# Kernel tuning notes

Measured on AMD Instinct MI355X. Metric: run time of the kernel, lower is better.

The kernel has to match this reference:

```python
import jax, jax.numpy as jnp
import numpy as np
from jax import lax

B, L, H = 256, 256, 128
K_MIN, K_MAX, ITERS = 2, 8, 3
ALPHA, BETA = 0.5, 0.5
EPS8, EPS9 = 1e-8, 1e-9


def setup_inputs() -> dict:
    key = jax.random.key(0)
    k1, k2, k3 = jax.random.split(key, 3)
    user_features = jax.random.normal(k1, (B, L, H), dtype=jnp.float32)
    W = jax.random.normal(k2, (H, H), dtype=jnp.float32) * (1.0 / np.sqrt(H))
    b_init = jax.random.normal(k3, (B, K_MAX, L), dtype=jnp.float32)
    return {"user_features": user_features, "W": W, "b_init": b_init}


def _cap_scale(cap):
    # squash-style scalar: n/(1+n)/sqrt(n+eps), n = ||cap||^2
    n = jnp.sum(cap * cap, axis=-1, keepdims=True)
    return n / (1.0 + n) / jnp.sqrt(n + EPS9)


def reference(user_features, W, b_init):
    e = user_features                                  # [B,L,H]
    hat = e @ W.T                                      # nn.Linear(H,H,bias=False)
    # repeat over capsules then transpose -> every capsule sees same projection
    hat_k = jnp.broadcast_to(hat[:, None, :, :], (B, K_MAX, L, H))
    hat_iter = lax.stop_gradient(hat_k)                # stop_grad=True path

    b = b_init
    cap = None
    c = None
    for t in range(ITERS):
        c = jax.nn.softmax(b, axis=-1)                 # mask is all ones
        if t < ITERS - 1:
            cap = jnp.einsum('bkl,bklh->bkh', c, hat_iter)
            cap = _cap_scale(cap) * cap
            delta = jnp.einsum('bklh,bkh->bkl', hat_iter, cap)
            b = b + delta
        else:
            cap = jnp.einsum('bkl,bklh->bkh', c, hat_k)
            cap = _cap_scale(cap) * cap
    interest_capsule = cap                             # [B,K,H]
    final_c = c                                        # [B,K,L]

    e_norm = e / (jnp.linalg.norm(e, axis=-1, keepdims=True) + EPS8)
    strength = jnp.linalg.norm(interest_capsule, axis=-1)  # [B,K]

    scores = []
    for k in range(K_MIN, K_MAX + 1):
        _, idx = lax.top_k(strength, k)                # [B,k]
        c_k = jnp.take_along_axis(final_c, idx[:, :, None], axis=1)  # [B,k,L]
        denom = c_k.sum(axis=-1, keepdims=True) + EPS8
        mu_k = jnp.einsum('bkl,blh->bkh', c_k, e) / denom
        mu_n = mu_k / (jnp.linalg.norm(mu_k, axis=-1, keepdims=True) + EPS8)
        cos = jnp.einsum('blh,bkh->bkl', e_norm, mu_n)
        consistency = (c_k * cos).sum(axis=(-1, -2)) / float(max(1, k) * max(1, L))
        if k > 1:
            pair = jnp.einsum('bkh,bjh->bkj', mu_n, mu_n)
            upper = jnp.triu(pair, k=1).sum(axis=(-1, -2))
            diversity = 1.0 - (2.0 / (k * (k - 1))) * upper
        else:
            diversity = jnp.ones((B,), dtype=mu_n.dtype)
        scores.append(ALPHA * consistency + BETA * diversity)

    k_scores = jnp.stack(scores, axis=1)               # [B, K_MAX-K_MIN+1]
    optimal_k = jnp.argmax(k_scores, axis=1) + K_MIN   # [B]
    return optimal_k, k_scores
```

## Files before the change

### kernel.cpp

```cpp
#include <hip/hip_runtime.h>
#include <hip/hip_bf16.h>
#include <math.h>

#define NB 256
#define NL 256
#define NH 128
#define NK 8

typedef __attribute__((ext_vector_type(8))) short bf16x8;
typedef __attribute__((ext_vector_type(4))) short s16x4;
typedef __attribute__((ext_vector_type(4))) float f32x4;

static __device__ __forceinline__ short f2bf(float x) {
    __hip_bfloat16 b = __float2bfloat16(x);
    return *reinterpret_cast<short*>(&b);
}
static __device__ __forceinline__ float bf2f(short s) {
    union { unsigned int u; float f; } v;
    v.u = ((unsigned int)(unsigned short)s) << 16;
    return v.f;
}

#define CTI(l, k) ((l) * 12 + ((((l) >> 5) & 7) << 2) + (k))
#define MFMA __builtin_amdgcn_mfma_f32_16x16x32_bf16

__global__ __launch_bounds__(256) void setup_w_kernel(const float* __restrict__ W,
                                                      short* __restrict__ whi,
                                                      short* __restrict__ wlo,
                                                      short* __restrict__ wthi,
                                                      short* __restrict__ wtlo) {
    const int id = blockIdx.x * 256 + threadIdx.x;
    const int h = id >> 7, j = id & 127;
    const float w = W[id];
    const short hi = f2bf(w);
    const short lo = f2bf(w - bf2f(hi));
    whi[id] = hi;
    wlo[id] = lo;
    wthi[j * 128 + h] = hi;
    wtlo[j * 128 + h] = lo;
}

__global__ __launch_bounds__(1024) void fused_kernel(const float* __restrict__ e,
                                                     const float* __restrict__ b_init,
                                                     const short* __restrict__ whi,
                                                     const short* __restrict__ wlo,
                                                     const short* __restrict__ wthi,
                                                     const short* __restrict__ wtlo,
                                                     float* __restrict__ out) {
    const int b = blockIdx.x;
    const int t = threadIdx.x;
    const int lane = t & 63, wv = t >> 6;
    const int l16 = lane & 15, grp = lane >> 4;

    __shared__ __align__(16) short ebx[NL * 264];
    __shared__ __align__(16) float ct12[3096];
    __shared__ __align__(16) short mpk[16 * 136];
    __shared__ __align__(16) short cappk[16 * 136];
    __shared__ __align__(16) short gpk[16 * 136];
    __shared__ float enl[256];
    __shared__ float red32[128];
    __shared__ float svals[8], strv[8], Ps[28];

    float* capb = (float*)gpk;

    const float* ebg = e + (size_t)b * (NL * NH);
#pragma unroll
    for (int rep = 0; rep < 8; ++rep) {
        const int idx4 = rep * 1024 + t;
        const int l = idx4 >> 5, c4 = idx4 & 31;
        const float4 v = *(const float4*)&ebg[l * 128 + c4 * 4];
        const float vx[4] = {v.x, v.y, v.z, v.w};
        s16x4 hv, lv;
        float ss = 0.f;
#pragma unroll
        for (int j = 0; j < 4; ++j) {
            const short h = f2bf(vx[j]);
            hv[j] = h;
            lv[j] = f2bf(vx[j] - bf2f(h));
            ss += vx[j] * vx[j];
        }
        *(s16x4*)&ebx[l * 264 + c4 * 8] = hv;
        *(s16x4*)&ebx[l * 264 + c4 * 8 + 4] = lv;
        ss += __shfl_xor(ss, 1); ss += __shfl_xor(ss, 2);
        ss += __shfl_xor(ss, 4); ss += __shfl_xor(ss, 8);
        ss += __shfl_xor(ss, 16);
        if ((lane & 31) == 0) enl[l] = sqrtf(ss) + 1e-8f;
    }

    float lr0 = 0.f, lr1 = 0.f, lr2 = 0.f, lr3 = 0.f;
    if (l16 < 8) {
        const float4 bi = *(const float4*)&b_init[(size_t)b * 2048 + l16 * 256 + wv * 16 + grp * 4];
        lr0 = bi.x; lr1 = bi.y; lr2 = bi.z; lr3 = bi.w;
    }
    __syncthreads();

    for (int iter = 0; iter < 3; ++iter) {
        {
            const float e0 = expf(lr0), e1 = expf(lr1);
            const float e2 = expf(lr2), e3 = expf(lr3);
            float s4 = e0 + e1 + e2 + e3;
            s4 += __shfl_xor(s4, 16);
            s4 += __shfl_xor(s4, 32);
            if (l16 < 8 && grp == 0) red32[wv * 8 + l16] = s4;
            __syncthreads();
            float ksum = 0.f;
#pragma unroll
            for (int w = 0; w < 16; ++w) ksum += red32[w * 8 + (l16 & 7)];
            const float inv = 1.0f / ksum;
            if (l16 < 8) {
                const int lb = wv * 16 + grp * 4;
                ct12[CTI(lb + 0, l16)] = e0 * inv;
                ct12[CTI(lb + 1, l16)] = e1 * inv;
                ct12[CTI(lb + 2, l16)] = e2 * inv;
                ct12[CTI(lb + 3, l16)] = e3 * inv;
            }
            __syncthreads();
        }

        {
            const int lm = lane & 31, khalf = lane >> 5;
            const int h8 = wv;
            float acc[4][8];
#pragma unroll
            for (int kq = 0; kq < 4; ++kq)
#pragma unroll
                for (int hh = 0; hh < 8; ++hh) acc[kq][hh] = 0.f;
#pragma unroll
            for (int i = 0; i < 8; ++i) {
                const int l = i * 32 + lm;
                const float4 cv = *(const float4*)&ct12[l * 12 + (((l >> 5) & 7) << 2) + khalf * 4];
                const bf16x8 r1 = *(const bf16x8*)&ebx[l * 264 + h8 * 16];
                const bf16x8 r2 = *(const bf16x8*)&ebx[l * 264 + h8 * 16 + 8];
                float ev[8];
#pragma unroll
                for (int j = 0; j < 4; ++j) {
                    ev[j] = bf2f(r1[j]) + bf2f(r1[4 + j]);
                    ev[4 + j] = bf2f(r2[j]) + bf2f(r2[4 + j]);
                }
                const float cvx[4] = {cv.x, cv.y, cv.z, cv.w};
#pragma unroll
                for (int kq = 0; kq < 4; ++kq)
#pragma unroll
                    for (int hh = 0; hh < 8; ++hh)
                        acc[kq][hh] += cvx[kq] * ev[hh];
            }
            float a1[16];
#pragma unroll
            for (int j = 0; j < 16; ++j) {
                const float keep = (lane & 1) ? acc[(2 * j + 1) >> 3][(2 * j + 1) & 7]
                                              : acc[(2 * j) >> 3][(2 * j) & 7];
                const float send = (lane & 1) ? acc[(2 * j) >> 3][(2 * j) & 7]
                                              : acc[(2 * j + 1) >> 3][(2 * j + 1) & 7];
                a1[j] = keep + __shfl_xor(send, 1);
            }
            float a2[8];
#pragma unroll
            for (int j = 0; j < 8; ++j) {
                const float keep = (lane & 2) ? a1[2 * j + 1] : a1[2 * j];
                const float send = (lane & 2) ? a1[2 * j] : a1[2 * j + 1];
                a2[j] = keep + __shfl_xor(send, 2);
            }
            float a3[4];
#pragma unroll
            for (int j = 0; j < 4; ++j) {
                const float keep = (lane & 4) ? a2[2 * j + 1] : a2[2 * j];
                const float send = (lane & 4) ? a2[2 * j] : a2[2 * j + 1];
                a3[j] = keep + __shfl_xor(send, 4);
            }
            float a4[2];
#pragma unroll
            for (int j = 0; j < 2; ++j) {
                const float keep = (lane & 8) ? a3[2 * j + 1] : a3[2 * j];
                const float send = (lane & 8) ? a3[2 * j] : a3[2 * j + 1];
                a4[j] = keep + __shfl_xor(send, 8);
            }
            const float keep5 = (lane & 16) ? a4[1] : a4[0];
            const float send5 = (lane & 16) ? a4[0] : a4[1];
            const float mval = keep5 + __shfl_xor(send5, 16);
            const int mk = khalf * 4 + ((lane & 31) >> 3);
            const int mo = mk * 136 + h8 * 8 + (lane & 7);
            const short mhv = f2bf(mval);
            mpk[mo] = mhv;
            mpk[(mk + 8) * 136 + mo - mk * 136] = f2bf(mval - bf2f(mhv));
        }
        __syncthreads();

        if (wv < 8) {
            const int n0 = wv * 16;
            f32x4 acc = (f32x4){0.f, 0.f, 0.f, 0.f};
#pragma unroll
            for (int ks = 0; ks < 4; ++ks) {
                const bf16x8 af = *(const bf16x8*)&mpk[l16 * 136 + ks * 32 + grp * 8];
                const int bo = (n0 + l16) * 128 + ks * 32 + grp * 8;
                acc = MFMA(af, *(const bf16x8*)&whi[bo], acc, 0, 0, 0);
                acc = MFMA(af, *(const bf16x8*)&wlo[bo], acc, 0, 0, 0);
            }
            f32x4 cs;
#pragma unroll
            for (int r = 0; r < 4; ++r) cs[r] = acc[r] + __shfl_xor(acc[r], 32);
            if (grp < 2) {
#pragma unroll
                for (int r = 0; r < 4; ++r)
                    capb[(grp * 4 + r) * 136 + n0 + l16] = cs[r];
            }
        }
        __syncthreads();

        if (wv < 8) {
            const int k = wv;
            float x0 = capb[k * 136 + lane], x1 = capb[k * 136 + 64 + lane];
            float s = x0 * x0 + x1 * x1;
#pragma unroll
            for (int o = 32; o; o >>= 1) s += __shfl_xor(s, o);
            const float sc = s / (1.0f + s) / sqrtf(s + 1e-9f);
            x0 *= sc; x1 *= sc;
            short hv = f2bf(x0);
            cappk[k * 136 + lane] = hv;
            cappk[(k + 8) * 136 + lane] = f2bf(x0 - bf2f(hv));
            hv = f2bf(x1);
            cappk[k * 136 + 64 + lane] = hv;
            cappk[(k + 8) * 136 + 64 + lane] = f2bf(x1 - bf2f(hv));
            if (iter == 2 && lane == 0)
                strv[k] = s / (1.0f + s) * sqrtf(s) / sqrtf(s + 1e-9f);
        }
        __syncthreads();

        if (iter < 2) {
            if (wv < 8) {
                const int n0 = wv * 16;
                f32x4 acc = (f32x4){0.f, 0.f, 0.f, 0.f};
#pragma unroll
                for (int ks = 0; ks < 4; ++ks) {
                    const bf16x8 af = *(const bf16x8*)&cappk[l16 * 136 + ks * 32 + grp * 8];
                    const int bo = (n0 + l16) * 128 + ks * 32 + grp * 8;
                    acc = MFMA(af, *(const bf16x8*)&wthi[bo], acc, 0, 0, 0);
                    acc = MFMA(af, *(const bf16x8*)&wtlo[bo], acc, 0, 0, 0);
                }
                f32x4 gs;
#pragma unroll
                for (int r = 0; r < 4; ++r) gs[r] = acc[r] + __shfl_xor(acc[r], 32);
                if (grp < 2) {
#pragma unroll
                    for (int r = 0; r < 4; ++r) {
                        const int k = grp * 4 + r, h = n0 + l16;
                        const short hv = f2bf(gs[r]);
                        gpk[k * 136 + h] = hv;
                        gpk[(k + 8) * 136 + h] = f2bf(gs[r] - bf2f(hv));
                    }
                }
            }
            __syncthreads();

            {
                const int m0 = wv * 16;
                f32x4 acc;
                acc[0] = (l16 < 8) ? lr0 : 0.f;
                acc[1] = (l16 < 8) ? lr1 : 0.f;
                acc[2] = (l16 < 8) ? lr2 : 0.f;
                acc[3] = (l16 < 8) ? lr3 : 0.f;
#pragma unroll
                for (int ks = 0; ks < 4; ++ks) {
                    const int eo = (m0 + l16) * 264 + ks * 64 + grp * 16;
                    const bf16x8 r1 = *(const bf16x8*)&ebx[eo];
                    const bf16x8 r2 = *(const bf16x8*)&ebx[eo + 8];
                    const bf16x8 ah = __builtin_shufflevector(r1, r2, 0, 1, 2, 3, 8, 9, 10, 11);
                    const bf16x8 al = __builtin_shufflevector(r1, r2, 4, 5, 6, 7, 12, 13, 14, 15);
                    const bf16x8 bf = *(const bf16x8*)&gpk[l16 * 136 + ks * 32 + grp * 8];
                    acc = MFMA(ah, bf, acc, 0, 0, 0);
                    acc = MFMA(al, bf, acc, 0, 0, 0);
                }
                lr0 = acc[0] + __shfl_xor(acc[0], 8);
                lr1 = acc[1] + __shfl_xor(acc[1], 8);
                lr2 = acc[2] + __shfl_xor(acc[2], 8);
                lr3 = acc[3] + __shfl_xor(acc[3], 8);
            }
        }
    }

    if (wv < 8) {
        const int k = wv;
        float x0 = bf2f(mpk[k * 136 + lane]) + bf2f(mpk[(k + 8) * 136 + lane]);
        float x1 = bf2f(mpk[k * 136 + 64 + lane]) + bf2f(mpk[(k + 8) * 136 + 64 + lane]);
        float s = x0 * x0 + x1 * x1;
#pragma unroll
        for (int o = 32; o; o >>= 1) s += __shfl_xor(s, o);
        const float nv = sqrtf(s) + 1e-8f;
        x0 /= nv; x1 /= nv;
        short hv = f2bf(x0);
        gpk[k * 136 + lane] = hv;
        gpk[(k + 8) * 136 + lane] = f2bf(x0 - bf2f(hv));
        hv = f2bf(x1);
        gpk[k * 136 + 64 + lane] = hv;
        gpk[(k + 8) * 136 + 64 + lane] = f2bf(x1 - bf2f(hv));
    }
    __syncthreads();

    {
        const int m0 = wv * 16;
        f32x4 acc = (f32x4){0.f, 0.f, 0.f, 0.f};
#pragma unroll
        for (int ks = 0; ks < 4; ++ks) {
            const int eo = (m0 + l16) * 264 + ks * 64 + grp * 16;
            const bf16x8 r1 = *(const bf16x8*)&ebx[eo];
            const bf16x8 r2 = *(const bf16x8*)&ebx[eo + 8];
            const bf16x8 ah = __builtin_shufflevector(r1, r2, 0, 1, 2, 3, 8, 9, 10, 11);
            const bf16x8 al = __builtin_shufflevector(r1, r2, 4, 5, 6, 7, 12, 13, 14, 15);
            const bf16x8 bf = *(const bf16x8*)&gpk[l16 * 136 + ks * 32 + grp * 8];
            acc = MFMA(ah, bf, acc, 0, 0, 0);
            acc = MFMA(al, bf, acc, 0, 0, 0);
        }
        f32x4 d;
#pragma unroll
        for (int r = 0; r < 4; ++r) d[r] = acc[r] + __shfl_xor(acc[r], 8);
        float sv = 0.f;
        if (l16 < 8) {
#pragma unroll
            for (int r = 0; r < 4; ++r) {
                const int l = m0 + grp * 4 + r;
                sv += d[r] * ct12[CTI(l, l16)] / enl[l];
            }
        }
        sv += __shfl_xor(sv, 16);
        sv += __shfl_xor(sv, 32);
        if (l16 < 8 && grp == 0) red32[wv * 8 + l16] = sv;
    }

#pragma unroll
    for (int pp = 0; pp < 2; ++pp) {
        const int p = wv + pp * 16;
        if (p < 28) {
            int i = 0, rem = p;
            while (rem >= 7 - i) { rem -= 7 - i; ++i; }
            const int j = i + 1 + rem;
            const float mi0 = bf2f(gpk[i * 136 + lane]) + bf2f(gpk[(i + 8) * 136 + lane]);
            const float mi1 = bf2f(gpk[i * 136 + 64 + lane]) + bf2f(gpk[(i + 8) * 136 + 64 + lane]);
            const float mj0 = bf2f(gpk[j * 136 + lane]) + bf2f(gpk[(j + 8) * 136 + lane]);
            const float mj1 = bf2f(gpk[j * 136 + 64 + lane]) + bf2f(gpk[(j + 8) * 136 + 64 + lane]);
            float v = mi0 * mj0 + mi1 * mj1;
#pragma unroll
            for (int o = 32; o; o >>= 1) v += __shfl_xor(v, o);
            if (lane == 0) Ps[p] = v;
        }
    }
    __syncthreads();
    if (t < 8) {
        float s = 0.f;
#pragma unroll
        for (int w = 0; w < 16; ++w) s += red32[w * 8 + t];
        svals[t] = s;
    }
    __syncthreads();

    if (t == 0) {
        int idx[8];
        for (int i = 0; i < 8; ++i) idx[i] = i;
        for (int a = 1; a < 8; ++a) {
            const int key = idx[a];
            const float kv = strv[key];
            int bb = a - 1;
            while (bb >= 0 && strv[idx[bb]] < kv) { idx[bb + 1] = idx[bb]; --bb; }
            idx[bb + 1] = key;
        }
        float best = -1e30f;
        int bestk = 2;
        float cons_sum = 0.f, pair_sum = 0.f;
        for (int kk = 1; kk <= 8; ++kk) {
            const int ni = idx[kk - 1];
            cons_sum += svals[ni];
            for (int a = 0; a < kk - 1; ++a) {
                const int ia = idx[a];
                const int lo = ia < ni ? ia : ni;
                const int hi2 = ia < ni ? ni : ia;
                const int off0 = lo * 7 - lo * (lo - 1) / 2;
                pair_sum += Ps[off0 + hi2 - lo - 1];
            }
            if (kk >= 2) {
                const float cons = cons_sum / (kk * 256.0f);
                const float divv = 1.0f - (2.0f / (kk * (kk - 1))) * pair_sum;
                const float score = 0.5f * cons + 0.5f * divv;
                out[256 + b * 7 + (kk - 2)] = score;
                if (score > best) { best = score; bestk = kk; }
            }
        }
        out[b] = (float)bestk;
    }
}

extern "C" void kernel_launch(void* const* d_in, const int* in_sizes, int n_in,
                              void* d_out, int out_size, void* d_ws, size_t ws_size,
                              hipStream_t stream) {
    const float* e = (const float*)d_in[0];
    const float* W = (const float*)d_in[1];
    const float* b_init = (const float*)d_in[2];
    float* out = (float*)d_out;

    short* whi = (short*)d_ws;
    short* wlo = whi + 16384;
    short* wthi = wlo + 16384;
    short* wtlo = wthi + 16384;

    hipLaunchKernelGGL(setup_w_kernel, dim3(64), dim3(256), 0, stream, W, whi, wlo, wthi, wtlo);
    hipLaunchKernelGGL(fused_kernel, dim3(NB), dim3(1024), 0, stream,
                       e, b_init, whi, wlo, wthi, wtlo, out);
}
```

Baseline: 46.43 us.

## Compute capsule weighted sums with MFMA over transposed split-bf16 features

New measurement: 39.54 us. 14.8% less time.

```diff
diff --git a/kernel.cpp b/kernel.cpp
--- a/kernel.cpp
+++ b/kernel.cpp
@@ -21,7 +21,6 @@
     return v.f;
 }
 
-#define CTI(l, k) ((l) * 12 + ((((l) >> 5) & 7) << 2) + (k))
 #define MFMA __builtin_amdgcn_mfma_f32_16x16x32_bf16
 
 __global__ __launch_bounds__(256) void setup_w_kernel(const float* __restrict__ W,
@@ -52,8 +51,9 @@
     const int lane = t & 63, wv = t >> 6;
     const int l16 = lane & 15, grp = lane >> 4;
 
-    __shared__ __align__(16) short ebx[NL * 264];
-    __shared__ __align__(16) float ct12[3096];
+    __shared__ __align__(16) short eThi[128 * 264];
+    __shared__ __align__(16) short eTlo[128 * 264];
+    __shared__ __align__(16) short cax[16 * 264];
     __shared__ __align__(16) short mpk[16 * 136];
     __shared__ __align__(16) short cappk[16 * 136];
     __shared__ __align__(16) short gpk[16 * 136];
@@ -64,27 +64,48 @@
     float* capb = (float*)gpk;
 
     const float* ebg = e + (size_t)b * (NL * NH);
-#pragma unroll
-    for (int rep = 0; rep < 8; ++rep) {
-        const int idx4 = rep * 1024 + t;
-        const int l = idx4 >> 5, c4 = idx4 & 31;
-        const float4 v = *(const float4*)&ebg[l * 128 + c4 * 4];
-        const float vx[4] = {v.x, v.y, v.z, v.w};
-        s16x4 hv, lv;
+
+    bf16x8 eah[4], eal[4];
+    {
+        const int row = wv * 16 + l16;
         float ss = 0.f;
 #pragma unroll
-        for (int j = 0; j < 4; ++j) {
-            const short h = f2bf(vx[j]);
-            hv[j] = h;
-            lv[j] = f2bf(vx[j] - bf2f(h));
-            ss += vx[j] * vx[j];
-        }
-        *(s16x4*)&ebx[l * 264 + c4 * 8] = hv;
-        *(s16x4*)&ebx[l * 264 + c4 * 8 + 4] = lv;
-        ss += __shfl_xor(ss, 1); ss += __shfl_xor(ss, 2);
-        ss += __shfl_xor(ss, 4); ss += __shfl_xor(ss, 8);
+        for (int ks = 0; ks < 4; ++ks) {
+            const float4 f0 = *(const float4*)&ebg[row * 128 + ks * 32 + grp * 8];
+            const float4 f1 = *(const float4*)&ebg[row * 128 + ks * 32 + grp * 8 + 4];
+            const float fx[8] = {f0.x, f0.y, f0.z, f0.w, f1.x, f1.y, f1.z, f1.w};
+            bf16x8 hv, lv;
+#pragma unroll
+            for (int j = 0; j < 8; ++j) {
+                const short h = f2bf(fx[j]);
+                hv[j] = h;
+                lv[j] = f2bf(fx[j] - bf2f(h));
+                ss += fx[j] * fx[j];
+            }
+            eah[ks] = hv;
+            eal[ks] = lv;
+        }
         ss += __shfl_xor(ss, 16);
-        if ((lane & 31) == 0) enl[l] = sqrtf(ss) + 1e-8f;
+        ss += __shfl_xor(ss, 32);
+        if (grp == 0) enl[wv * 16 + l16] = sqrtf(ss) + 1e-8f;
+    }
+
+#pragma unroll
+    for (int i = 0; i < 4; ++i) {
+        const int p = i * 1024 + t;
+        const int h = p & 127, c = p >> 7;
+        float le[8];
+#pragma unroll
+        for (int j = 0; j < 8; ++j) le[j] = ebg[(c * 8 + j) * 128 + h];
+        bf16x8 hv, lv;
+#pragma unroll
+        for (int j = 0; j < 8; ++j) {
+            const short s = f2bf(le[j]);
+            hv[j] = s;
+            lv[j] = f2bf(le[j] - bf2f(s));
+        }
+        *(bf16x8*)&eThi[h * 264 + c * 8] = hv;
+        *(bf16x8*)&eTlo[h * 264 + c * 8] = lv;
     }
 
     float lr0 = 0.f, lr1 = 0.f, lr2 = 0.f, lr3 = 0.f;
@@ -109,79 +130,43 @@
             const float inv = 1.0f / ksum;
             if (l16 < 8) {
                 const int lb = wv * 16 + grp * 4;
-                ct12[CTI(lb + 0, l16)] = e0 * inv;
-                ct12[CTI(lb + 1, l16)] = e1 * inv;
-                ct12[CTI(lb + 2, l16)] = e2 * inv;
-                ct12[CTI(lb + 3, l16)] = e3 * inv;
+                const float cv[4] = {e0 * inv, e1 * inv, e2 * inv, e3 * inv};
+                s16x4 his, los;
+#pragma unroll
+                for (int j = 0; j < 4; ++j) {
+                    const short h = f2bf(cv[j]);
+                    his[j] = h;
+                    los[j] = f2bf(cv[j] - bf2f(h));
+                }
+                *(s16x4*)&cax[l16 * 264 + lb] = his;
+                *(s16x4*)&cax[(l16 + 8) * 264 + lb] = los;
             }
             __syncthreads();
         }
 
-        {
-            const int lm = lane & 31, khalf = lane >> 5;
-            const int h8 = wv;
-            float acc[4][8];
-#pragma unroll
-            for (int kq = 0; kq < 4; ++kq)
-#pragma unroll
-                for (int hh = 0; hh < 8; ++hh) acc[kq][hh] = 0.f;
-#pragma unroll
-            for (int i = 0; i < 8; ++i) {
-                const int l = i * 32 + lm;
-                const float4 cv = *(const float4*)&ct12[l * 12 + (((l >> 5) & 7) << 2) + khalf * 4];
-                const bf16x8 r1 = *(const bf16x8*)&ebx[l * 264 + h8 * 16];
-                const bf16x8 r2 = *(const bf16x8*)&ebx[l * 264 + h8 * 16 + 8];
-                float ev[8];
-#pragma unroll
-                for (int j = 0; j < 4; ++j) {
-                    ev[j] = bf2f(r1[j]) + bf2f(r1[4 + j]);
-                    ev[4 + j] = bf2f(r2[j]) + bf2f(r2[4 + j]);
-                }
-                const float cvx[4] = {cv.x, cv.y, cv.z, cv.w};
-#pragma unroll
-                for (int kq = 0; kq < 4; ++kq)
-#pragma unroll
-                    for (int hh = 0; hh < 8; ++hh)
-                        acc[kq][hh] += cvx[kq] * ev[hh];
-            }
-            float a1[16];
-#pragma unroll
-            for (int j = 0; j < 16; ++j) {
-                const float keep = (lane & 1) ? acc[(2 * j + 1) >> 3][(2 * j + 1) & 7]
-                                              : acc[(2 * j) >> 3][(2 * j) & 7];
-                const float send = (lane & 1) ? acc[(2 * j) >> 3][(2 * j) & 7]
-                                              : acc[(2 * j + 1) >> 3][(2 * j + 1) & 7];
-                a1[j] = keep + __shfl_xor(send, 1);
-            }
-            float a2[8];
-#pragma unroll
-            for (int j = 0; j < 8; ++j) {
-                const float keep = (lane & 2) ? a1[2 * j + 1] : a1[2 * j];
-                const float send = (lane & 2) ? a1[2 * j] : a1[2 * j + 1];
-                a2[j] = keep + __shfl_xor(send, 2);
-            }
-            float a3[4];
-#pragma unroll
-            for (int j = 0; j < 4; ++j) {
-                const float keep = (lane & 4) ? a2[2 * j + 1] : a2[2 * j];
-                const float send = (lane & 4) ? a2[2 * j] : a2[2 * j + 1];
-                a3[j] = keep + __shfl_xor(send, 4);
-            }
-            float a4[2];
-#pragma unroll
-            for (int j = 0; j < 2; ++j) {
-                const float keep = (lane & 8) ? a3[2 * j + 1] : a3[2 * j];
-                const float send = (lane & 8) ? a3[2 * j] : a3[2 * j + 1];
-                a4[j] = keep + __shfl_xor(send, 8);
-            }
-            const float keep5 = (lane & 16) ? a4[1] : a4[0];
-            const float send5 = (lane & 16) ? a4[0] : a4[1];
-            const float mval = keep5 + __shfl_xor(send5, 16);
-            const int mk = khalf * 4 + ((lane & 31) >> 3);
-            const int mo = mk * 136 + h8 * 8 + (lane & 7);
-            const short mhv = f2bf(mval);
-            mpk[mo] = mhv;
-            mpk[(mk + 8) * 136 + mo - mk * 136] = f2bf(mval - bf2f(mhv));
+        if (wv < 8) {
+            const int n0 = wv * 16;
+            f32x4 acc = (f32x4){0.f, 0.f, 0.f, 0.f};
+#pragma unroll
+            for (int ks = 0; ks < 8; ++ks) {
+                const bf16x8 af = *(const bf16x8*)&cax[l16 * 264 + ks * 32 + grp * 8];
+                const bf16x8 bh = *(const bf16x8*)&eThi[(n0 + l16) * 264 + ks * 32 + grp * 8];
+                const bf16x8 bl = *(const bf16x8*)&eTlo[(n0 + l16) * 264 + ks * 32 + grp * 8];
+                acc = MFMA(af, bh, acc, 0, 0, 0);
+                acc = MFMA(af, bl, acc, 0, 0, 0);
+            }
+            f32x4 ms;
+#pragma unroll
+            for (int r = 0; r < 4; ++r) ms[r] = acc[r] + __shfl_xor(acc[r], 32);
+            if (grp < 2) {
+#pragma unroll
+                for (int r = 0; r < 4; ++r) {
+                    const int k = grp * 4 + r, h = n0 + l16;
+                    const short hv = f2bf(ms[r]);
+                    mpk[k * 136 + h] = hv;
+                    mpk[(k + 8) * 136 + h] = f2bf(ms[r] - bf2f(hv));
+                }
+            }
         }
         __syncthreads();
 
@@ -252,7 +237,6 @@
             __syncthreads();
 
             {
-                const int m0 = wv * 16;
                 f32x4 acc;
                 acc[0] = (l16 < 8) ? lr0 : 0.f;
                 acc[1] = (l16 < 8) ? lr1 : 0.f;
@@ -260,14 +244,9 @@
                 acc[3] = (l16 < 8) ? lr3 : 0.f;
 #pragma unroll
                 for (int ks = 0; ks < 4; ++ks) {
-                    const int eo = (m0 + l16) * 264 + ks * 64 + grp * 16;
-                    const bf16x8 r1 = *(const bf16x8*)&ebx[eo];
-                    const bf16x8 r2 = *(const bf16x8*)&ebx[eo + 8];
-                    const bf16x8 ah = __builtin_shufflevector(r1, r2, 0, 1, 2, 3, 8, 9, 10, 11);
-                    const bf16x8 al = __builtin_shufflevector(r1, r2, 4, 5, 6, 7, 12, 13, 14, 15);
                     const bf16x8 bf = *(const bf16x8*)&gpk[l16 * 136 + ks * 32 + grp * 8];
-                    acc = MFMA(ah, bf, acc, 0, 0, 0);
-                    acc = MFMA(al, bf, acc, 0, 0, 0);
+                    acc = MFMA(eah[ks], bf, acc, 0, 0, 0);
+                    acc = MFMA(eal[ks], bf, acc, 0, 0, 0);
                 }
                 lr0 = acc[0] + __shfl_xor(acc[0], 8);
                 lr1 = acc[1] + __shfl_xor(acc[1], 8);
@@ -296,18 +275,12 @@
     __syncthreads();
 
     {
-        const int m0 = wv * 16;
         f32x4 acc = (f32x4){0.f, 0.f, 0.f, 0.f};
 #pragma unroll
         for (int ks = 0; ks < 4; ++ks) {
-            const int eo = (m0 + l16) * 264 + ks * 64 + grp * 16;
-            const bf16x8 r1 = *(const bf16x8*)&ebx[eo];
-            const bf16x8 r2 = *(const bf16x8*)&ebx[eo + 8];
-            const bf16x8 ah = __builtin_shufflevector(r1, r2, 0, 1, 2, 3, 8, 9, 10, 11);
-            const bf16x8 al = __builtin_shufflevector(r1, r2, 4, 5, 6, 7, 12, 13, 14, 15);
             const bf16x8 bf = *(const bf16x8*)&gpk[l16 * 136 + ks * 32 + grp * 8];
-            acc = MFMA(ah, bf, acc, 0, 0, 0);
-            acc = MFMA(al, bf, acc, 0, 0, 0);
+            acc = MFMA(eah[ks], bf, acc, 0, 0, 0);
+            acc = MFMA(eal[ks], bf, acc, 0, 0, 0);
         }
         f32x4 d;
 #pragma unroll
@@ -316,8 +289,9 @@
         if (l16 < 8) {
 #pragma unroll
             for (int r = 0; r < 4; ++r) {
-                const int l = m0 + grp * 4 + r;
-                sv += d[r] * ct12[CTI(l, l16)] / enl[l];
+                const int l = wv * 16 + grp * 4 + r;
+                const float cv = bf2f(cax[l16 * 264 + l]) + bf2f(cax[(l16 + 8) * 264 + l]);
+                sv += d[r] * cv / enl[l];
             }
         }
         sv += __shfl_xor(sv, 16);
```
